# Kernel tuning notes

Hardware: AMD Instinct MI355X
Metric: run time of the kernel (lower is better)

## Reference

```python
import jax, jax.numpy as jnp
import numpy as np

B, T, N, C = 32, 12, 1024, 2   # batch, lookback window, n_series, in_channels
D, H, K, OUT = 16, 64, 2, 12   # embedding_dim, rnn_units, cheb_k, out_dim (horizon)


def setup_inputs() -> dict:
    key = jax.random.key(0)
    ks = jax.random.split(key, 12)
    p = lambda k, sh, s=0.1: jax.random.normal(k, sh, dtype=jnp.float32) * s
    return {
        "source": jax.random.normal(ks[0], (B, T, N, C), dtype=jnp.float32),
        "node_emb": p(ks[1], (N, D), 0.3),
        # layer 0: dim_in = C + H
        "gate_w0": p(ks[2], (D, K, C + H, 2 * H)),
        "gate_b0": p(ks[3], (D, 2 * H)),
        "upd_w0": p(ks[4], (D, K, C + H, H)),
        "upd_b0": p(ks[5], (D, H)),
        # layer 1: dim_in = H + H
        "gate_w1": p(ks[6], (D, K, 2 * H, 2 * H)),
        "gate_b1": p(ks[7], (D, 2 * H)),
        "upd_w1": p(ks[8], (D, K, 2 * H, H)),
        "upd_b1": p(ks[9], (D, H)),
        # end_conv: Conv2d(1, OUT*out_channels, kernel=(1,H)) == linear over hidden dim
        "conv_w": p(ks[10], (OUT, H)),
        "conv_b": p(ks[11], (OUT,)),
    }


def _supports(node_emb):
    # softmax(relu(E E^T)) row-normalized adaptive adjacency; Chebyshev stack (K, N, N)
    A = jax.nn.softmax(jax.nn.relu(node_emb @ node_emb.T), axis=1)
    s = [jnp.eye(N, dtype=A.dtype), A]
    for _ in range(2, K):
        s.append(2.0 * A @ s[-1] - s[-2])
    return jnp.stack(s, axis=0)


def _gcn(x, node_emb, w_pool, b_pool, supports):
    # x: (B, N, Cin); per-node adaptive weights from pools
    w = jnp.einsum('nd,dkio->nkio', node_emb, w_pool)     # (N, K, Cin, Cout)
    b = node_emb @ b_pool                                 # (N, Cout)
    xg = jnp.einsum('knm,bmc->bnkc', supports, x)         # (B, N, K, Cin)
    return jnp.einsum('bnki,nkio->bno', xg, w) + b


def _layer(x_seq, node_emb, supports, gw, gb, uw, ub):
    # x_seq: (B, T, N, Cin) -> (B, T, N, H) via GRU-style AGCRN cell, scanned over T
    def step(state, x_t):
        inp = jnp.concatenate([x_t, state], axis=-1)
        zr = jax.nn.sigmoid(_gcn(inp, node_emb, gw, gb, supports))
        z, r = jnp.split(zr, 2, axis=-1)
        cand = jnp.concatenate([x_t, z * state], axis=-1)
        hc = jnp.tanh(_gcn(cand, node_emb, uw, ub, supports))
        h = r * state + (1.0 - r) * hc
        return h, h

    init = jnp.zeros((x_seq.shape[0], N, H), dtype=x_seq.dtype)
    _, hs = jax.lax.scan(step, init, jnp.swapaxes(x_seq, 0, 1))
    return jnp.swapaxes(hs, 0, 1)


def reference(source, node_emb, gate_w0, gate_b0, upd_w0, upd_b0,
              gate_w1, gate_b1, upd_w1, upd_b1, conv_w, conv_b,
              teacher_forcing_ratio=0):
    sup = _supports(node_emb)  # adaptive supports depend only on static node_emb
    h1 = _layer(source, node_emb, sup, gate_w0, gate_b0, upd_w0, upd_b0)
    h2 = _layer(h1, node_emb, sup, gate_w1, gate_b1, upd_w1, upd_b1)
    last = h2[:, -1]  # (B, N, H)
    # end_conv over hidden dim -> (B, OUT, N); out_channels==1 so squeeze folds away
    out = jnp.einsum('bnh,oh->bon', last, conv_w) + conv_b[None, :, None]
    return out
```

## Files before the change

### kernel.cpp

```cpp
#include <hip/hip_runtime.h>
#include <hip/hip_fp16.h>


typedef _Float16 f16x8 __attribute__((ext_vector_type(8)));
typedef _Float16 f16x4 __attribute__((ext_vector_type(4)));
typedef float f32x4 __attribute__((ext_vector_type(4)));

#define WAIT_VM0 asm volatile("s_waitcnt vmcnt(0)" ::: "memory")
#define WAIT_VM1 asm volatile("s_waitcnt vmcnt(1)" ::: "memory")
#define WAIT_VM2 asm volatile("s_waitcnt vmcnt(2)" ::: "memory")
#define WAIT_VM1_LG asm volatile("s_waitcnt vmcnt(1) lgkmcnt(0)" ::: "memory")
#define WAIT_VM2_LG asm volatile("s_waitcnt vmcnt(2) lgkmcnt(0)" ::: "memory")
#define WAIT_LG asm volatile("s_waitcnt lgkmcnt(0)" ::: "memory")
#define BARRIER do { __builtin_amdgcn_s_barrier(); asm volatile("" ::: "memory"); } while (0)

__device__ __forceinline__ void gload_lds16(const void* g, void* l) {
  __builtin_amdgcn_global_load_lds(
      (const __attribute__((address_space(1))) void*)g,
      (__attribute__((address_space(3))) void*)l, 16, 0, 0);
}

__device__ __forceinline__ void dma_g128(const _Float16* Wc, _Float16* buf, int tid) {
  int wave = tid >> 6;
#pragma unroll
  for (int u = 0; u < 2; ++u) {
    gload_lds16(Wc + (size_t)(u * 256 + tid) * 8,
                buf + (size_t)(u * 256 + wave * 64) * 8);
  }
}

__device__ __forceinline__ void dma_g64(const _Float16* Wc, _Float16* buf, int tid) {
  int wave = tid >> 6;
  gload_lds16(Wc + (size_t)tid * 8, buf + (size_t)(wave * 64) * 8);
}

__device__ __forceinline__ f16x8 wrd(const _Float16* buf, int o, int s) {
  int flat = (o & 7) | (((s ^ (o & 3)) & 3) << 3) | ((o >> 3) << 5);
  return *(const f16x8*)(buf + flat * 8);
}

__global__ __launch_bounds__(256) void compute_A_kernel(const float* __restrict__ E,
                                                        __half* __restrict__ Ah) {
  int n = blockIdx.x;
  int tid = threadIdx.x;
  __shared__ float red[256];
  float en[16];
#pragma unroll
  for (int d = 0; d < 16; ++d) en[d] = E[n * 16 + d];
  float v[4];
#pragma unroll
  for (int q = 0; q < 4; ++q) {
    int m = tid + q * 256;
    const float* Em = E + m * 16;
    float dot = 0.f;
#pragma unroll
    for (int d = 0; d < 16; ++d) dot += en[d] * Em[d];
    v[q] = fmaxf(dot, 0.f);
  }
  float mx = fmaxf(fmaxf(v[0], v[1]), fmaxf(v[2], v[3]));
  red[tid] = mx; __syncthreads();
  for (int s = 128; s > 0; s >>= 1) { if (tid < s) red[tid] = fmaxf(red[tid], red[tid + s]); __syncthreads(); }
  mx = red[0];
  __syncthreads();
  float e[4], sum = 0.f;
#pragma unroll
  for (int q = 0; q < 4; ++q) { e[q] = expf(v[q] - mx); sum += e[q]; }
  red[tid] = sum; __syncthreads();
  for (int s = 128; s > 0; s >>= 1) { if (tid < s) red[tid] += red[tid + s]; __syncthreads(); }
  float inv = 1.f / red[0];
#pragma unroll
  for (int q = 0; q < 4; ++q) Ah[(size_t)n * 1024 + tid + q * 256] = __float2half(e[q] * inv);
}

__global__ __launch_bounds__(256) void pool_t16_kernel(const float* __restrict__ gw0,
                                                       const float* __restrict__ uw0,
                                                       const float* __restrict__ gw1,
                                                       const float* __restrict__ uw1,
                                                       __half* __restrict__ poolT16) {
  int rg = blockIdx.x;
  const float* pool; int F, Fp, O; size_t jbase; int kk, jj;
  if (rg < 160)      { pool = gw0; F = 66;  Fp = 80;  O = 128; jbase = 0;     kk = rg / 80;          jj = rg % 80; }
  else if (rg < 320) { pool = uw0; F = 66;  Fp = 80;  O = 64;  jbase = 20480; kk = (rg - 160) / 80;  jj = (rg - 160) % 80; }
  else if (rg < 576) { pool = gw1; F = 128; Fp = 128; O = 128; jbase = 30720; kk = (rg - 320) / 128; jj = (rg - 320) % 128; }
  else               { pool = uw1; F = 128; Fp = 128; O = 64;  jbase = 63488; kk = (rg - 576) / 128; jj = (rg - 576) % 128; }
  int o = threadIdx.x;
  if (o >= O) return;
  int i;
  if (F == Fp) i = jj;
  else i = (jj < 64) ? jj + 2 : (jj < 66 ? jj - 64 : -1);
  f16x8 a = {}, b = {}, zz = {};
  if (i >= 0) {
#pragma unroll
    for (int d = 0; d < 8; ++d)
      a[d] = (_Float16)pool[(((size_t)d * 2 + kk) * F + i) * O + o];
#pragma unroll
    for (int d = 8; d < 16; ++d)
      b[d - 8] = (_Float16)pool[(((size_t)d * 2 + kk) * F + i) * O + o];
  }
  size_t j = jbase + (size_t)o * (2 * Fp) + (size_t)kk * Fp + jj;
  _Float16* outp = (_Float16*)poolT16 + j * 32;
  *(f16x8*)outp = a;
  *(f16x8*)(outp + 8) = b;
  *(f16x8*)(outp + 16) = zz;
  *(f16x8*)(outp + 24) = zz;
}

__global__ __launch_bounds__(256) void prelude_misc_kernel(
    const float* __restrict__ E, __half* __restrict__ E16,
    const float* __restrict__ gb0, const float* __restrict__ ub0,
    const float* __restrict__ gb1, const float* __restrict__ ub1,
    float* __restrict__ Bg0, float* __restrict__ Bu0,
    float* __restrict__ Bg1, float* __restrict__ Bu1,
    const float* __restrict__ src, __half* __restrict__ x16,
    float4* __restrict__ zero_p) {
  int bid = blockIdx.x;
  if (bid < 8192) {
    int i = bid * 256 + threadIdx.x;
    zero_p[i] = float4{0.f, 0.f, 0.f, 0.f};
    return;
  }
  bid -= 8192;
  if (bid < 384) {
    int t0 = bid >> 5, b = bid & 31;
    const float* s = src + (size_t)(b * 12 + t0) * 2048;
    __half* dst = x16 + t0 * 64 + b * 2;
    for (int nn = threadIdx.x; nn < 1024; nn += 256) {
      float2 v = *(const float2*)(s + nn * 2);
      *(__half2*)(dst + (size_t)nn * 768) = __floats2half2_rn(v.x, v.y);
    }
    return;
  }
  bid -= 384;
  if (bid < 1536) {
    int tid = bid * 256 + threadIdx.x;
    if (tid >= 1024 * 384) return;
    int n = tid / 384, c = tid - n * 384;
    const float* pool; float* outp; int O, o;
    if (c < 128)      { pool = gb0; outp = Bg0; O = 128; o = c; }
    else if (c < 192) { pool = ub0; outp = Bu0; O = 64;  o = c - 128; }
    else if (c < 320) { pool = gb1; outp = Bg1; O = 128; o = c - 192; }
    else              { pool = ub1; outp = Bu1; O = 64;  o = c - 320; }
    const float* En = E + n * 16;
    float a = 0.f;
#pragma unroll
    for (int d = 0; d < 16; ++d) a += En[d] * pool[d * O + o];
    outp[n * O + o] = a;
    return;
  }
  bid -= 1536;
  {
    int t = bid * 256 + threadIdx.x;
    if (t >= 1024 * 32) return;
    int d = t & 31;
    E16[t] = (d < 16) ? __float2half(E[(t >> 5) * 16 + d]) : __half(0);
  }
}

__global__ __launch_bounds__(256) void make_wt_mfma_kernel(
    const __half* __restrict__ E16g, const __half* __restrict__ poolT16g,
    __half* __restrict__ WtG0, __half* __restrict__ WtU0,
    __half* __restrict__ WtG1, __half* __restrict__ WtU1) {
  __shared__ __align__(16) _Float16 Es[64][40];
  __shared__ __align__(16) _Float16 wbuf[64][264];
  const _Float16* E16 = (const _Float16*)E16g;
  const _Float16* pT = (const _Float16*)poolT16g;
  int bx = blockIdx.x;
  __half* Wt; int O, KIP, segbase, kc, og;
  if (bx < 80)       { Wt = WtG0; O = 128; KIP = 160; segbase = 0;     kc = bx % 5;          og = bx / 5; }
  else if (bx < 120) { Wt = WtU0; O = 64;  KIP = 160; segbase = 20480; kc = (bx - 80) % 5;   og = (bx - 80) / 5; }
  else if (bx < 248) { Wt = WtG1; O = 128; KIP = 256; segbase = 30720; kc = (bx - 120) % 8;  og = (bx - 120) / 8; }
  else               { Wt = WtU1; O = 64;  KIP = 256; segbase = 63488; kc = (bx - 248) % 8;  og = (bx - 248) / 8; }
  int o0 = og * 8;
  int n0 = blockIdx.y * 64;
  {
    int r = threadIdx.x >> 2, ch = (threadIdx.x & 3) * 8;
    *(f16x8*)&Es[r][ch] = *(const f16x8*)(E16 + (size_t)(n0 + r) * 32 + ch);
  }
  __syncthreads();
  int wave = threadIdx.x >> 6, lane = threadIdx.x & 63;
  int fm = lane & 15, fg = lane >> 4;
  f16x8 af[4];
#pragma unroll
  for (int i = 0; i < 4; ++i) af[i] = *(const f16x8*)&Es[i * 16 + fm][fg * 8];
  f32x4 acc[4][4] = {};
#pragma unroll
  for (int jt = 0; jt < 4; ++jt) {
    int local = wave * 64 + jt * 16 + fm;
    int oo = local >> 5, kip = local & 31;
    size_t jc = (size_t)segbase + (size_t)(o0 + oo) * KIP + kc * 32 + kip;
    f16x8 bf = *(const f16x8*)(pT + jc * 32 + fg * 8);
#pragma unroll
    for (int i = 0; i < 4; ++i)
      acc[i][jt] = __builtin_amdgcn_mfma_f32_16x16x32_f16(af[i], bf, acc[i][jt], 0, 0, 0);
  }
#pragma unroll
  for (int i = 0; i < 4; ++i)
#pragma unroll
    for (int jt = 0; jt < 4; ++jt)
#pragma unroll
      for (int r = 0; r < 4; ++r)
        wbuf[i * 16 + fg * 4 + r][wave * 64 + jt * 16 + fm] = (_Float16)acc[i][jt][r];
  __syncthreads();
  int NCH = KIP >> 5;
  int CH = O * 32;
  int sbase = (o0 >> 3) * 256;
  for (int idx = threadIdx.x; idx < 64 * 32; idx += 256) {
    int nsub = idx >> 5, w = idx & 31;
    int oo = w & 7;
    int s = (w >> 3) ^ (w & 3);
    int pos = oo * 32 + s * 8;
    size_t dst = ((size_t)(n0 + nsub) * NCH + kc) * CH + sbase + (size_t)w * 8;
    *(float4*)(Wt + dst) = *(float4*)&wbuf[nsub][pos];
  }
}

__global__ __launch_bounds__(256) void gemm_nt_kernel(
    const __half* __restrict__ Ahg, const __half* __restrict__ X0g,
    const __half* __restrict__ X1g, __half* __restrict__ Yg,
    int Nc, int cstride, int split) {
  __shared__ __align__(16) _Float16 As[64][136];
  __shared__ __align__(16) _Float16 Bs[64][144];
  const _Float16* __restrict__ Ah = (const _Float16*)Ahg;
  _Float16* __restrict__ Y = (_Float16*)Yg;
  int tid = threadIdx.x;
  int row0 = blockIdx.y * 64;
  int col0 = blockIdx.x * 64;
  const _Float16* __restrict__ Xsrc =
      (col0 < split) ? (const _Float16*)X0g : (const _Float16*)X1g;
  int colg = (col0 < split) ? col0 : col0 - split;
  int wave = tid >> 6, lane = tid & 63;
  int wm = wave & 1, wn = wave >> 1;
  int fm = lane & 15, fg = lane >> 4;

  int sr = tid >> 2, sc = (tid & 3) * 32;
  const _Float16* pa = Ah + (size_t)(row0 + sr) * 1024 + sc;
  int kq = tid & 31, cg = tid >> 5;
  int kb = 4 * kq;
  const _Float16* pb = Xsrc + (size_t)kb * cstride + colg + cg * 8;
  int chunk = kq >> 1;
  int kin = (kq & 1) * 4;

  f16x8 ra[4], rb[4];
#pragma unroll
  for (int c = 0; c < 4; ++c) ra[c] = *(const f16x8*)(pa + c * 8);
#pragma unroll
  for (int r = 0; r < 4; ++r) rb[r] = *(const f16x8*)(pb + (size_t)r * cstride);

  f32x4 acc[2][2] = {};
  for (int k0 = 0; k0 < 1024; k0 += 128) {
#pragma unroll
    for (int c = 0; c < 4; ++c) *(f16x8*)&As[sr][sc + c * 8] = ra[c];
#pragma unroll
    for (int i = 0; i < 8; ++i) {
      int c = cg * 8 + i;
// ... 68 lines not shown
  int kin = (kq & 1) * 4;

  f16x8 ra[4], rb[4][2];
#pragma unroll
  for (int c = 0; c < 4; ++c) ra[c] = *(const f16x8*)(pa + c * 8);
#pragma unroll
  for (int r = 0; r < 4; ++r)
#pragma unroll
    for (int h = 0; h < 2; ++h)
      rb[r][h] = *(const f16x8*)(pb + (size_t)r * cstride + h * 8);

  f32x4 acc[4][2] = {};
  for (int k0 = 0; k0 < 1024; k0 += 128) {
#pragma unroll
    for (int c = 0; c < 4; ++c) *(f16x8*)&As[sr][sc + c * 8] = ra[c];
#pragma unroll
    for (int h = 0; h < 2; ++h)
#pragma unroll
      for (int i = 0; i < 8; ++i) {
        int c = cg * 16 + h * 8 + i;
        f16x4 p;
        p[0] = rb[0][h][i]; p[1] = rb[1][h][i]; p[2] = rb[2][h][i]; p[3] = rb[3][h][i];
        *(f16x4*)&Bs[c][((chunk ^ (c & 7)) << 3) + kin] = p;
      }
    __syncthreads();
    if (k0 + 128 < 1024) {
#pragma unroll
      for (int c = 0; c < 4; ++c) ra[c] = *(const f16x8*)(pa + k0 + 128 + c * 8);
#pragma unroll
      for (int r = 0; r < 4; ++r)
#pragma unroll
        for (int h = 0; h < 2; ++h)
          rb[r][h] = *(const f16x8*)(pb + (size_t)(k0 + 128 + r) * cstride + h * 8);
    }
#pragma unroll
    for (int kc = 0; kc < 4; ++kc) {
      int ck = kc * 4 + fg;
      f16x8 af[4], bf[2];
#pragma unroll
      for (int i = 0; i < 4; ++i)
        af[i] = *(const f16x8*)&As[i * 16 + fm][kc * 32 + fg * 8];
#pragma unroll
      for (int j = 0; j < 2; ++j) {
        int cl = wave * 32 + j * 16 + fm;
        bf[j] = *(const f16x8*)&Bs[cl][(ck ^ (cl & 7)) << 3];
      }
#pragma unroll
      for (int i = 0; i < 4; ++i)
#pragma unroll
        for (int j = 0; j < 2; ++j)
          acc[i][j] = __builtin_amdgcn_mfma_f32_16x16x32_f16(af[i], bf[j], acc[i][j], 0, 0, 0);
    }
    __syncthreads();
  }
#pragma unroll
  for (int i = 0; i < 4; ++i) {
#pragma unroll
    for (int j = 0; j < 2; ++j) {
      int col = col0 + wave * 32 + j * 16 + fm;
      int rbase = row0 + i * 16 + fg * 4;
#pragma unroll
      for (int r = 0; r < 4; ++r)
        Y[(size_t)(rbase + r) * Nc + col] = (_Float16)acc[i][j][r];
    }
  }
}

__device__ __forceinline__ f16x8 ld_g0(const __half* __restrict__ h16,
                                       const __half* __restrict__ YBD, int n, int idx) {
  int b = idx >> 4, part = (idx >> 3) & 1, ch = idx & 7;
  const _Float16* s = part ? (const _Float16*)YBD + (size_t)n * 4096 + b * 64 + ch * 8
                           : (const _Float16*)h16 + (size_t)n * 2048 + b * 64 + ch * 8;
  return *(const f16x8*)s;
}
__device__ __forceinline__ f16x8 ld_u0(const __half* __restrict__ zh0,
                                       const __half* __restrict__ YCE, int n, int idx) {
  int b = idx >> 4, part = (idx >> 3) & 1, ch = idx & 7;
  const _Float16* s = part ? (const _Float16*)YCE + (size_t)n * 4096 + 2048 + b * 64 + ch * 8
                           : (const _Float16*)zh0 + (size_t)n * 2048 + b * 64 + ch * 8;
  return *(const f16x8*)s;
}

__device__ __forceinline__ void gate0_body(
    _Float16* Xs, _Float16 (*Wb)[4096], int n, int t,
    f16x8 pre0, f16x8 pre1, float2 xv, unsigned axu,
    const _Float16* Wn, const float* __restrict__ Bg,
    const float* __restrict__ h32, __half* __restrict__ zh0, __half* __restrict__ r0) {
  constexpr int STRIDE = 168;
  {
    int b0 = t >> 4, p0 = (t >> 3) & 1, c0 = t & 7;
    *(f16x8*)&Xs[b0 * STRIDE + p0 * 80 + c0 * 8] = pre0;
    int idx = t + 256;
    int b1 = idx >> 4, p1 = (idx >> 3) & 1, c1 = idx & 7;
    *(f16x8*)&Xs[b1 * STRIDE + p1 * 80 + c1 * 8] = pre1;
  }
  if (t < 32) {
    Xs[t * STRIDE + 64] = (_Float16)xv.x;
    Xs[t * STRIDE + 65] = (_Float16)xv.y;
    *(unsigned*)&Xs[t * STRIDE + 144] = axu;
  }
  for (int idx = t; idx < 896; idx += 256) {
    int b = idx / 28, jj = idx % 28;
    int col = (jj < 14) ? 66 + jj : 132 + jj;
    Xs[b * STRIDE + col] = (_Float16)0.f;
  }
  int wave = t >> 6, lane = t & 63;
  int fm = lane & 15, fg = lane >> 4;
  f32x4 acc[2][2] = {};
#pragma unroll
  for (int kc = 0; kc < 5; ++kc) {
    if (kc == 0) WAIT_VM2_LG;
    else if (kc < 4) WAIT_VM2;
    else WAIT_VM0;
    BARRIER;
    const _Float16* wb = Wb[kc & 1];
    f16x8 af[2], bf[2];
#pragma unroll
    for (int i = 0; i < 2; ++i)
      af[i] = *(const f16x8*)&Xs[(i * 16 + fm) * STRIDE + kc * 32 + fg * 8];
#pragma unroll
    for (int j = 0; j < 2; ++j)
      bf[j] = wrd(wb, wave * 32 + j * 16 + fm, fg);
    WAIT_LG;
    BARRIER;
    if (kc < 3) dma_g128(Wn + (size_t)(kc + 2) * 4096, Wb[kc & 1], t);
    __builtin_amdgcn_s_setprio(1);
#pragma unroll
    for (int i = 0; i < 2; ++i)
#pragma unroll
      for (int j = 0; j < 2; ++j)
        acc[i][j] = __builtin_amdgcn_mfma_f32_16x16x32_f16(af[i], bf[j], acc[i][j], 0, 0, 0);
    __builtin_amdgcn_s_setprio(0);
  }
  const float* Bn = Bg + n * 128;
#pragma unroll
  for (int j = 0; j < 2; ++j) {
    int o = wave * 32 + j * 16 + fm;
    float bias = Bn[o];
#pragma unroll
    for (int i = 0; i < 2; ++i)
#pragma unroll
      for (int r = 0; r < 4; ++r) {
        int b = i * 16 + fg * 4 + r;
        float s = 1.f / (1.f + __expf(-(acc[i][j][r] + bias)));
        size_t base = (size_t)n * 2048 + b * 64;
        if (o < 64) zh0[base + o] = __float2half(s * h32[base + o]);
        else        r0[base + o - 64] = __float2half(s);
      }
  }
}

__device__ __forceinline__ void upd0_body(
    _Float16* Xs, _Float16 (*Wb)[4096], int n, int t,
    f16x8 pre0, f16x8 pre1, float2 xv, unsigned axu,
    const _Float16* Wn, const float* __restrict__ Bu,
    const __half* __restrict__ r0, float* __restrict__ h32, __half* __restrict__ h16) {
  constexpr int STRIDE = 168;
  {
    int b0 = t >> 4, p0 = (t >> 3) & 1, c0 = t & 7;
    *(f16x8*)&Xs[b0 * STRIDE + p0 * 80 + c0 * 8] = pre0;
    int idx = t + 256;
    int b1 = idx >> 4, p1 = (idx >> 3) & 1, c1 = idx & 7;
    *(f16x8*)&Xs[b1 * STRIDE + p1 * 80 + c1 * 8] = pre1;
  }
  if (t < 32) {
    Xs[t * STRIDE + 64] = (_Float16)xv.x;
    Xs[t * STRIDE + 65] = (_Float16)xv.y;
    *(unsigned*)&Xs[t * STRIDE + 144] = axu;
  }
  for (int idx = t; idx < 896; idx += 256) {
    int b = idx / 28, jj = idx % 28;
    int col = (jj < 14) ? 66 + jj : 132 + jj;
    Xs[b * STRIDE + col] = (_Float16)0.f;
  }
  int wave = t >> 6, lane = t & 63;
  int fm = lane & 15, fg = lane >> 4;
  f32x4 acc[2] = {};
#pragma unroll
  for (int kc = 0; kc < 5; ++kc) {
    if (kc == 0) WAIT_VM1_LG;
    else if (kc < 4) WAIT_VM1;
    else WAIT_VM0;
    BARRIER;
    const _Float16* wb = Wb[kc & 1];
    f16x8 bf = wrd(wb, wave * 16 + fm, fg);
    f16x8 af0 = *(const f16x8*)&Xs[(0 * 16 + fm) * STRIDE + kc * 32 + fg * 8];
    f16x8 af1 = *(const f16x8*)&Xs[(1 * 16 + fm) * STRIDE + kc * 32 + fg * 8];
    WAIT_LG;
    BARRIER;
    if (kc < 3) dma_g64(Wn + (size_t)(kc + 2) * 2048, Wb[kc & 1], t);
    __builtin_amdgcn_s_setprio(1);
    acc[0] = __builtin_amdgcn_mfma_f32_16x16x32_f16(af0, bf, acc[0], 0, 0, 0);
    acc[1] = __builtin_amdgcn_mfma_f32_16x16x32_f16(af1, bf, acc[1], 0, 0, 0);
    __builtin_amdgcn_s_setprio(0);
  }
  int o = wave * 16 + fm;
  float bias = Bu[n * 64 + o];
#pragma unroll
  for (int i = 0; i < 2; ++i)
#pragma unroll
    for (int r = 0; r < 4; ++r) {
      int b = i * 16 + fg * 4 + r;
      float x = acc[i][r] + bias;
      x = fminf(fmaxf(x, -15.f), 15.f);
      float e = __expf(2.f * x);
      float hc = (e - 1.f) / (e + 1.f);
      size_t base = (size_t)n * 2048 + b * 64;
      float rr = __half2float(r0[base + o]);
      float hnew = rr * h32[base + o] + (1.f - rr) * hc;
      h32[base + o] = hnew;
      h16[base + o] = __float2half(hnew);
    }
}

__global__ __launch_bounds__(256) void gate0_kernel(
    const __half* __restrict__ h16, const __half* __restrict__ YBD,
    const float* __restrict__ src, const __half* __restrict__ Axt, int tstep,
    const __half* __restrict__ Wtg, const float* __restrict__ Bg,
    const float* __restrict__ h32, __half* __restrict__ zh0, __half* __restrict__ r0) {
  __shared__ __align__(16) _Float16 Xs[32 * 168];
  __shared__ __align__(16) _Float16 Wb[2][4096];
  int n = blockIdx.x, t = threadIdx.x;
  const _Float16* Wn = (const _Float16*)Wtg + (size_t)n * 20480;
  f16x8 p0 = ld_g0(h16, YBD, n, t);
  f16x8 p1 = ld_g0(h16, YBD, n, t + 256);
  float2 xv = {}; unsigned ax = 0;
  if (t < 32) {
    xv = *(const float2*)(src + ((size_t)(t * 12 + tstep) * 1024 + n) * 2);
    ax = *(const unsigned*)((const _Float16*)Axt + (size_t)n * 768 + tstep * 64 + t * 2);
  }
  dma_g128(Wn, Wb[0], t);
  dma_g128(Wn + 4096, Wb[1], t);
  gate0_body(Xs, Wb, n, t, p0, p1, xv, ax, Wn, Bg, h32, zh0, r0);
}

__global__ __launch_bounds__(256) void upd0_kernel(
    const __half* __restrict__ zh0, const __half* __restrict__ YCE,
    const float* __restrict__ src, const __half* __restrict__ Axt, int tstep,
    const __half* __restrict__ Wtg, const float* __restrict__ Bu,
    const __half* __restrict__ r0, float* __restrict__ h32, __half* __restrict__ h16) {
  __shared__ __align__(16) _Float16 Xs[32 * 168];
  __shared__ __align__(16) _Float16 Wb[2][4096];
  int n = blockIdx.x, t = threadIdx.x;
  const _Float16* Wn = (const _Float16*)Wtg + (size_t)n * 10240;
  f16x8 p0 = ld_u0(zh0, YCE, n, t);
  f16x8 p1 = ld_u0(zh0, YCE, n, t + 256);
  float2 xv = {}; unsigned ax = 0;
  if (t < 32) {
    xv = *(const float2*)(src + ((size_t)(t * 12 + tstep) * 1024 + n) * 2);
    ax = *(const unsigned*)((const _Float16*)Axt + (size_t)n * 768 + tstep * 64 + t * 2);
  }
  dma_g64(Wn, Wb[0], t);
  dma_g64(Wn + 2048, Wb[1], t);
  upd0_body(Xs, Wb, n, t, p0, p1, xv, ax, Wn, Bu, r0, h32, h16);
}

__global__ __launch_bounds__(256) void gate1_gate0_kernel(
    const __half* __restrict__ h1_16, const __half* __restrict__ h2_16,
    const __half* __restrict__ YBD,
    const __half* __restrict__ WtG1, const float* __restrict__ Bg1,
    const float* __restrict__ h2_32, __half* __restrict__ zh1, __half* __restrict__ r1,
    const float* __restrict__ src, const __half* __restrict__ Axt, int tnext,
    const __half* __restrict__ WtG0, const float* __restrict__ Bg0,
    const float* __restrict__ h1_32, __half* __restrict__ zh0, __half* __restrict__ r0,
    int do_gate0) {
  constexpr int STRIDE = 264;
  __shared__ __align__(16) _Float16 Xs[32 * STRIDE];
  __shared__ __align__(16) _Float16 Wb[2][4096];
  int n = blockIdx.x;
  int t = threadIdx.x;
  const _Float16* Wn1 = (const _Float16*)WtG1 + (size_t)n * 32768;
  const _Float16* Wn0 = (const _Float16*)WtG0 + (size_t)n * 20480;
  f16x8 s1[4];
#pragma unroll
  for (int u = 0; u < 4; ++u) {
    int idx = t + u * 256;
    int b = idx >> 5, q = idx & 31;
    const _Float16* s;
    if (q < 8)       s = (const _Float16*)h1_16 + (size_t)n * 2048 + b * 64 + q * 8;
    else if (q < 16) s = (const _Float16*)h2_16 + (size_t)n * 2048 + b * 64 + (q - 8) * 8;
    else if (q < 24) s = (const _Float16*)YBD + (size_t)n * 4096 + b * 64 + (q - 16) * 8;
    else             s = (const _Float16*)YBD + (size_t)n * 4096 + 2048 + b * 64 + (q - 24) * 8;
    s1[u] = *(const f16x8*)s;
  }
  f16x8 g0p0 = {}, g0p1 = {}; float2 g0xv = {}; unsigned g0ax = 0;
  if (do_gate0) {
    g0p0 = ld_g0(h1_16, YBD, n, t);
    g0p1 = ld_g0(h1_16, YBD, n, t + 256);
    if (t < 32) {
      g0xv = *(const float2*)(src + ((size_t)(t * 12 + tnext) * 1024 + n) * 2);
      g0ax = *(const unsigned*)((const _Float16*)Axt + (size_t)n * 768 + tnext * 64 + t * 2);
    }
  }
  dma_g128(Wn1, Wb[0], t);
  dma_g128(Wn1 + 4096, Wb[1], t);
#pragma unroll
  for (int u = 0; u < 4; ++u) {
    int idx = t + u * 256;
    int b = idx >> 5, q = idx & 31;
    *(f16x8*)&Xs[b * STRIDE + q * 8] = s1[u];
  }
  int wave = t >> 6, lane = t & 63;
  int fm = lane & 15, fg = lane >> 4;
  {
    f32x4 acc[2][2] = {};
#pragma unroll
    for (int kc = 0; kc < 8; ++kc) {
      if (kc == 0) WAIT_VM2_LG;
      else if (kc < 7) WAIT_VM2;
      else { if (do_gate0) WAIT_VM2; else WAIT_VM0; }
      BARRIER;
      const _Float16* wb = Wb[kc & 1];
      f16x8 af[2], bf[2];
#pragma unroll
      for (int i = 0; i < 2; ++i)
        af[i] = *(const f16x8*)&Xs[(i * 16 + fm) * STRIDE + kc * 32 + fg * 8];
#pragma unroll
      for (int j = 0; j < 2; ++j)
        bf[j] = wrd(wb, wave * 32 + j * 16 + fm, fg);
      WAIT_LG;
      BARRIER;
      if (kc < 6) dma_g128(Wn1 + (size_t)(kc + 2) * 4096, Wb[kc & 1], t);
      else if (do_gate0) dma_g128(Wn0 + (size_t)(kc - 6) * 4096, Wb[kc & 1], t);
      __builtin_amdgcn_s_setprio(1);
#pragma unroll
      for (int i = 0; i < 2; ++i)
#pragma unroll
        for (int j = 0; j < 2; ++j)
          acc[i][j] = __builtin_amdgcn_mfma_f32_16x16x32_f16(af[i], bf[j], acc[i][j], 0, 0, 0);
      __builtin_amdgcn_s_setprio(0);
    }
    const float* Bn = Bg1 + n * 128;
#pragma unroll
    for (int j = 0; j < 2; ++j) {
      int o = wave * 32 + j * 16 + fm;
      float bias = Bn[o];
#pragma unroll
      for (int i = 0; i < 2; ++i)
#pragma unroll
        for (int r = 0; r < 4; ++r) {
          int b = i * 16 + fg * 4 + r;
          float s = 1.f / (1.f + __expf(-(acc[i][j][r] + bias)));
          size_t base = (size_t)n * 2048 + b * 64;
          if (o < 64) zh1[base + o] = __float2half(s * h2_32[base + o]);
          else        r1[base + o - 64] = __float2half(s);
        }
    }
  }
  if (!do_gate0) return;
  gate0_body(Xs, Wb, n, t, g0p0, g0p1, g0xv, g0ax, Wn0, Bg0, h1_32, zh0, r0);
}

__global__ __launch_bounds__(256) void upd1_upd0_kernel(
    const __half* __restrict__ h1_16, const __half* __restrict__ zh1,
    const __half* __restrict__ YBD, const __half* __restrict__ YCE,
    const __half* __restrict__ WtU1, const float* __restrict__ Bu1,
    const __half* __restrict__ r1, float* __restrict__ h2_32, __half* __restrict__ h2_16,
    const __half* __restrict__ zh0,
    const float* __restrict__ src, const __half* __restrict__ Axt, int tnext,
    const __half* __restrict__ WtU0, const float* __restrict__ Bu0,
    const __half* __restrict__ r0, float* __restrict__ h1_32, __half* __restrict__ h1_16w,
    int do_upd0) {
  constexpr int STRIDE = 264;
  __shared__ __align__(16) _Float16 Xs[32 * STRIDE];
  __shared__ __align__(16) _Float16 Wb[2][4096];
  int n = blockIdx.x;
  int t = threadIdx.x;
  const _Float16* Wn1 = (const _Float16*)WtU1 + (size_t)n * 16384;
  const _Float16* Wn0 = (const _Float16*)WtU0 + (size_t)n * 10240;
  f16x8 s1[4];
#pragma unroll
  for (int u = 0; u < 4; ++u) {
    int idx = t + u * 256;
    int b = idx >> 5, q = idx & 31;
    const _Float16* s;
    if (q < 8)       s = (const _Float16*)h1_16 + (size_t)n * 2048 + b * 64 + q * 8;
    else if (q < 16) s = (const _Float16*)zh1 + (size_t)n * 2048 + b * 64 + (q - 8) * 8;
    else if (q < 24) s = (const _Float16*)YBD + (size_t)n * 4096 + b * 64 + (q - 16) * 8;
    else             s = (const _Float16*)YCE + (size_t)n * 4096 + b * 64 + (q - 24) * 8;
    s1[u] = *(const f16x8*)s;
  }
  f16x8 u0p0 = {}, u0p1 = {}; float2 u0xv = {}; unsigned u0ax = 0;
  if (do_upd0) {
    u0p0 = ld_u0(zh0, YCE, n, t);
    u0p1 = ld_u0(zh0, YCE, n, t + 256);
    if (t < 32) {
      u0xv = *(const float2*)(src + ((size_t)(t * 12 + tnext) * 1024 + n) * 2);
      u0ax = *(const unsigned*)((const _Float16*)Axt + (size_t)n * 768 + tnext * 64 + t * 2);
    }
  }
  dma_g64(Wn1, Wb[0], t);
  dma_g64(Wn1 + 2048, Wb[1], t);
#pragma unroll
  for (int u = 0; u < 4; ++u) {
    int idx = t + u * 256;
    int b = idx >> 5, q = idx & 31;
    *(f16x8*)&Xs[b * STRIDE + q * 8] = s1[u];
  }
  int wave = t >> 6, lane = t & 63;
  int fm = lane & 15, fg = lane >> 4;
  {
    f32x4 acc[2] = {};
#pragma unroll
    for (int kc = 0; kc < 8; ++kc) {
      if (kc == 0) WAIT_VM1_LG;
      else if (kc < 7) WAIT_VM1;
      else { if (do_upd0) WAIT_VM1; else WAIT_VM0; }
      BARRIER;
      const _Float16* wb = Wb[kc & 1];
      f16x8 bf = wrd(wb, wave * 16 + fm, fg);
      f16x8 af0 = *(const f16x8*)&Xs[(0 * 16 + fm) * STRIDE + kc * 32 + fg * 8];
      f16x8 af1 = *(const f16x8*)&Xs[(1 * 16 + fm) * STRIDE + kc * 32 + fg * 8];
      WAIT_LG;
      BARRIER;
      if (kc < 6) dma_g64(Wn1 + (size_t)(kc + 2) * 2048, Wb[kc & 1], t);
      else if (do_upd0) dma_g64(Wn0 + (size_t)(kc - 6) * 2048, Wb[kc & 1], t);
      __builtin_amdgcn_s_setprio(1);
      acc[0] = __builtin_amdgcn_mfma_f32_16x16x32_f16(af0, bf, acc[0], 0, 0, 0);
      acc[1] = __builtin_amdgcn_mfma_f32_16x16x32_f16(af1, bf, acc[1], 0, 0, 0);
      __builtin_amdgcn_s_setprio(0);
    }
    int o = wave * 16 + fm;
    float bias = Bu1[n * 64 + o];
#pragma unroll
    for (int i = 0; i < 2; ++i)
#pragma unroll
      for (int r = 0; r < 4; ++r) {
        int b = i * 16 + fg * 4 + r;
        float x = acc[i][r] + bias;
        x = fminf(fmaxf(x, -15.f), 15.f);
        float e = __expf(2.f * x);
        float hc = (e - 1.f) / (e + 1.f);
        size_t base = (size_t)n * 2048 + b * 64;
        float rr = __half2float(r1[base + o]);
        float hnew = rr * h2_32[base + o] + (1.f - rr) * hc;
        h2_32[base + o] = hnew;
        h2_16[base + o] = __float2half(hnew);
      }
  }
  if (!do_upd0) return;
  upd0_body(Xs, Wb, n, t, u0p0, u0p1, u0xv, u0ax, Wn0, Bu0, r0, h1_32, h1_16w);
}

__global__ void final_conv_kernel(const float* __restrict__ h2, const float* __restrict__ cw,
                                  const float* __restrict__ cb, float* __restrict__ out) {
  int tid = blockIdx.x * 256 + threadIdx.x;
  if (tid >= 32 * 1024) return;
  int n = tid & 1023, b = tid >> 10;
  const float* hp = h2 + ((size_t)n * 32 + b) * 64;
  float hv[64];
#pragma unroll
  for (int i = 0; i < 64; ++i) hv[i] = hp[i];
#pragma unroll
  for (int o = 0; o < 12; ++o) {
    float acc = cb[o];
#pragma unroll
    for (int i = 0; i < 64; ++i) acc += hv[i] * cw[o * 64 + i];
    out[((size_t)b * 12 + o) * 1024 + n] = acc;
  }
}

extern "C" void kernel_launch(void* const* d_in, const int* in_sizes, int n_in,
                              void* d_out, int out_size, void* d_ws, size_t ws_size,
                              hipStream_t stream) {
  const float* src = (const float*)d_in[0];
  const float* E   = (const float*)d_in[1];
  const float* gw0 = (const float*)d_in[2];
  const float* gb0 = (const float*)d_in[3];
  const float* uw0 = (const float*)d_in[4];
  const float* ub0 = (const float*)d_in[5];
  const float* gw1 = (const float*)d_in[6];
  const float* gb1 = (const float*)d_in[7];
  const float* uw1 = (const float*)d_in[8];
  const float* ub1 = (const float*)d_in[9];
  const float* cw  = (const float*)d_in[10];
  const float* cb  = (const float*)d_in[11];
  float* out = (float*)d_out;
  (void)in_sizes; (void)n_in; (void)out_size; (void)ws_size;

  char* base = (char*)d_ws;
  size_t off = 0;
  auto alloc = [&](size_t bytes) -> void* {
    void* p = base + off; off += (bytes + 511) & ~(size_t)511; return p;
  };
  __half* Ah   = (__half*)alloc((size_t)1024 * 1024 * 2);
  __half* WtG0 = (__half*)alloc((size_t)1024 * 128 * 160 * 2);
  __half* WtU0 = (__half*)alloc((size_t)1024 * 64 * 160 * 2);
  __half* WtG1 = (__half*)alloc((size_t)1024 * 128 * 256 * 2);
  __half* WtU1 = (__half*)alloc((size_t)1024 * 64 * 256 * 2);
  float*  Bg0  = (float*) alloc((size_t)1024 * 128 * 4);
  float*  Bu0  = (float*) alloc((size_t)1024 * 64 * 4);
  float*  Bg1  = (float*) alloc((size_t)1024 * 128 * 4);
  float*  Bu1  = (float*) alloc((size_t)1024 * 64 * 4);
  float*  h1_32 = (float*)alloc((size_t)1024 * 2048 * 4);
  float*  h2_32 = (float*)alloc((size_t)1024 * 2048 * 4);
  __half* h1_16 = (__half*)alloc((size_t)1024 * 2048 * 2);
  __half* h2_16 = (__half*)alloc((size_t)1024 * 2048 * 2);
  __half* YBD  = (__half*)alloc((size_t)1024 * 4096 * 2);
  __half* YCE  = (__half*)alloc((size_t)1024 * 4096 * 2);
  __half* zh0  = (__half*)alloc((size_t)1024 * 2048 * 2);
  __half* zh1  = (__half*)alloc((size_t)1024 * 2048 * 2);
  __half* Axt  = (__half*)alloc((size_t)1024 * 768 * 2);
  __half* r1   = (__half*)alloc((size_t)1024 * 2048 * 2);
  __half* r0   = (__half*)alloc((size_t)1024 * 2048 * 2);
  __half* poolT16 = (__half*)alloc((size_t)79872 * 32 * 2);
  __half* E16  = (__half*)alloc((size_t)1024 * 32 * 2);
  __half* x16  = (__half*)alloc((size_t)1024 * 768 * 2);

  compute_A_kernel<<<1024, 256, 0, stream>>>(E, Ah);
  prelude_misc_kernel<<<10240, 256, 0, stream>>>(E, E16, gb0, ub0, gb1, ub1,
                                                 Bg0, Bu0, Bg1, Bu1,
                                                 src, x16, (float4*)h1_32);
  pool_t16_kernel<<<832, 256, 0, stream>>>(gw0, uw0, gw1, uw1, poolT16);
  make_wt_mfma_kernel<<<dim3(312, 16), 256, 0, stream>>>(E16, poolT16, WtG0, WtU0, WtG1, WtU1);
  gemm_nt_kernel<<<dim3(12, 16), 256, 0, stream>>>(Ah, (__half*)x16, (__half*)x16, Axt,
                                                   768, 768, 768);

  gate0_kernel<<<1024, 256, 0, stream>>>(h1_16, YBD, src, Axt, 0, WtG0, Bg0, h1_32, zh0, r0);
  gemm_nt128_kernel<<<dim3(16, 16), 256, 0, stream>>>(Ah, zh0, zh0, YCE + 2048,
                                                      4096, 2048, 2048);
  upd0_kernel<<<1024, 256, 0, stream>>>(zh0, YCE, src, Axt, 0, WtU0, Bu0, r0, h1_32, h1_16);

  for (int t = 0; t < 12; ++t) {
    int more = (t < 11) ? 1 : 0;
    gemm_nt128_kernel<<<dim3(32, 16), 256, 0, stream>>>(Ah, h1_16, h2_16, YBD,
                                                        4096, 2048, 2048);
    gate1_gate0_kernel<<<1024, 256, 0, stream>>>(h1_16, h2_16, YBD, WtG1, Bg1, h2_32, zh1, r1,
                                                 src, Axt, t + 1, WtG0, Bg0, h1_32, zh0, r0,
                                                 more);
    gemm_nt128_kernel<<<dim3(32, 16), 256, 0, stream>>>(Ah, zh1, zh0, YCE,
                                                        4096, 2048, 2048);
    upd1_upd0_kernel<<<1024, 256, 0, stream>>>(h1_16, zh1, YBD, YCE, WtU1, Bu1, r1,
                                               h2_32, h2_16, zh0, src, Axt, t + 1,
                                               WtU0, Bu0, r0, h1_32, h1_16, more);
  }

  final_conv_kernel<<<(32 * 1024 + 255) / 256, 256, 0, stream>>>(h2_32, cw, cb, out);
}
```

Baseline: 1.343 ms.

## Split layer-0 input-channel terms out of MFMA into scalar epilogue FMAs

```diff
diff --git a/kernel.cpp b/kernel.cpp
--- a/kernel.cpp
+++ b/kernel.cpp
@@ -78,26 +78,21 @@
                                                        const float* __restrict__ uw1,
                                                        __half* __restrict__ poolT16) {
   int rg = blockIdx.x;
-  const float* pool; int F, Fp, O; size_t jbase; int kk, jj;
-  if (rg < 160)      { pool = gw0; F = 66;  Fp = 80;  O = 128; jbase = 0;     kk = rg / 80;          jj = rg % 80; }
-  else if (rg < 320) { pool = uw0; F = 66;  Fp = 80;  O = 64;  jbase = 20480; kk = (rg - 160) / 80;  jj = (rg - 160) % 80; }
-  else if (rg < 576) { pool = gw1; F = 128; Fp = 128; O = 128; jbase = 30720; kk = (rg - 320) / 128; jj = (rg - 320) % 128; }
-  else               { pool = uw1; F = 128; Fp = 128; O = 64;  jbase = 63488; kk = (rg - 576) / 128; jj = (rg - 576) % 128; }
+  const float* pool; int F, O, TK; size_t jb; int kk, jj, i;
+  if (rg < 128)      { pool = gw0; F = 66;  O = 128; TK = 64;  jb = 0;     kk = rg >> 6; jj = rg & 63; i = jj + 2; }
+  else if (rg < 256) { int r = rg - 128; pool = uw0; F = 66;  O = 64;  TK = 64;  jb = 16384; kk = r >> 6; jj = r & 63;  i = jj + 2; }
+  else if (rg < 512) { int r = rg - 256; pool = gw1; F = 128; O = 128; TK = 128; jb = 24576; kk = r >> 7; jj = r & 127; i = jj; }
+  else               { int r = rg - 512; pool = uw1; F = 128; O = 64;  TK = 128; jb = 57344; kk = r >> 7; jj = r & 127; i = jj; }
   int o = threadIdx.x;
   if (o >= O) return;
-  int i;
-  if (F == Fp) i = jj;
-  else i = (jj < 64) ? jj + 2 : (jj < 66 ? jj - 64 : -1);
-  f16x8 a = {}, b = {}, zz = {};
-  if (i >= 0) {
-#pragma unroll
-    for (int d = 0; d < 8; ++d)
-      a[d] = (_Float16)pool[(((size_t)d * 2 + kk) * F + i) * O + o];
-#pragma unroll
-    for (int d = 8; d < 16; ++d)
-      b[d - 8] = (_Float16)pool[(((size_t)d * 2 + kk) * F + i) * O + o];
-  }
-  size_t j = jbase + (size_t)o * (2 * Fp) + (size_t)kk * Fp + jj;
+  f16x8 a, b, zz = {};
+#pragma unroll
+  for (int d = 0; d < 8; ++d)
+    a[d] = (_Float16)pool[(((size_t)d * 2 + kk) * F + i) * O + o];
+#pragma unroll
+  for (int d = 8; d < 16; ++d)
+    b[d - 8] = (_Float16)pool[(((size_t)d * 2 + kk) * F + i) * O + o];
+  size_t j = jb + (size_t)o * (2 * TK) + (size_t)kk * TK + jj;
   _Float16* outp = (_Float16*)poolT16 + j * 32;
   *(f16x8*)outp = a;
   *(f16x8*)(outp + 8) = b;
@@ -112,6 +107,8 @@
     float* __restrict__ Bg0, float* __restrict__ Bu0,
     float* __restrict__ Bg1, float* __restrict__ Bu1,
     const float* __restrict__ src, __half* __restrict__ x16,
+    const float* __restrict__ gw0, const float* __restrict__ uw0,
+    float* __restrict__ WxG0, float* __restrict__ WxU0,
     float4* __restrict__ zero_p) {
   int bid = blockIdx.x;
   if (bid < 8192) {
@@ -148,11 +145,36 @@
     return;
   }
   bid -= 1536;
-  {
+  if (bid < 128) {
     int t = bid * 256 + threadIdx.x;
-    if (t >= 1024 * 32) return;
     int d = t & 31;
     E16[t] = (d < 16) ? __float2half(E[(t >> 5) * 16 + d]) : __half(0);
+    return;
+  }
+  bid -= 128;
+  if (bid < 2048) {
+    int v = bid * 256 + threadIdx.x;
+    int n = v >> 9, q = (v >> 7) & 3, o = v & 127;
+    int kk = q >> 1, c = q & 1;
+    const float* En = E + n * 16;
+    float a = 0.f;
+#pragma unroll
+    for (int d = 0; d < 16; ++d)
+      a += En[d] * gw0[(((size_t)d * 2 + kk) * 66 + c) * 128 + o];
+    WxG0[(size_t)n * 512 + q * 128 + o] = __half2float(__float2half(a));
+    return;
+  }
+  bid -= 2048;
+  {
+    int v = bid * 256 + threadIdx.x;
+    int n = v >> 8, q = (v >> 6) & 3, o = v & 63;
+    int kk = q >> 1, c = q & 1;
+    const float* En = E + n * 16;
+    float a = 0.f;
+#pragma unroll
+    for (int d = 0; d < 16; ++d)
+      a += En[d] * uw0[(((size_t)d * 2 + kk) * 66 + c) * 64 + o];
+    WxU0[(size_t)n * 256 + q * 64 + o] = __half2float(__float2half(a));
   }
 }
 
@@ -166,10 +188,10 @@
   const _Float16* pT = (const _Float16*)poolT16g;
   int bx = blockIdx.x;
   __half* Wt; int O, KIP, segbase, kc, og;
-  if (bx < 80)       { Wt = WtG0; O = 128; KIP = 160; segbase = 0;     kc = bx % 5;          og = bx / 5; }
-  else if (bx < 120) { Wt = WtU0; O = 64;  KIP = 160; segbase = 20480; kc = (bx - 80) % 5;   og = (bx - 80) / 5; }
-  else if (bx < 248) { Wt = WtG1; O = 128; KIP = 256; segbase = 30720; kc = (bx - 120) % 8;  og = (bx - 120) / 8; }
-  else               { Wt = WtU1; O = 64;  KIP = 256; segbase = 63488; kc = (bx - 248) % 8;  og = (bx - 248) / 8; }
+  if (bx < 64)       { Wt = WtG0; O = 128; KIP = 128; segbase = 0;     kc = bx & 3;  og = bx >> 2; }
+  else if (bx < 96)  { int b = bx - 64;  Wt = WtU0; O = 64;  KIP = 128; segbase = 16384; kc = b & 3; og = b >> 2; }
+  else if (bx < 224) { int b = bx - 96;  Wt = WtG1; O = 128; KIP = 256; segbase = 24576; kc = b & 7; og = b >> 3; }
+  else               { int b = bx - 224; Wt = WtU1; O = 64;  KIP = 256; segbase = 57344; kc = b & 7; og = b >> 3; }
   int o0 = og * 8;
   int n0 = blockIdx.y * 64;
   {
@@ -404,35 +426,32 @@
 }
 
 __device__ __forceinline__ void gate0_body(
-    _Float16* Xs, _Float16 (*Wb)[4096], int n, int t,
+    _Float16* Xs, float (*xq)[4], _Float16 (*Wb)[4096], int n, int t,
     f16x8 pre0, f16x8 pre1, float2 xv, unsigned axu,
-    const _Float16* Wn, const float* __restrict__ Bg,
+    const _Float16* Wn, const float* __restrict__ Bg, const float* __restrict__ Wxg,
     const float* __restrict__ h32, __half* __restrict__ zh0, __half* __restrict__ r0) {
-  constexpr int STRIDE = 168;
+  constexpr int STRIDE = 136;
   {
     int b0 = t >> 4, p0 = (t >> 3) & 1, c0 = t & 7;
-    *(f16x8*)&Xs[b0 * STRIDE + p0 * 80 + c0 * 8] = pre0;
+    *(f16x8*)&Xs[b0 * STRIDE + p0 * 64 + c0 * 8] = pre0;
     int idx = t + 256;
     int b1 = idx >> 4, p1 = (idx >> 3) & 1, c1 = idx & 7;
-    *(f16x8*)&Xs[b1 * STRIDE + p1 * 80 + c1 * 8] = pre1;
+    *(f16x8*)&Xs[b1 * STRIDE + p1 * 64 + c1 * 8] = pre1;
   }
   if (t < 32) {
-    Xs[t * STRIDE + 64] = (_Float16)xv.x;
-    Xs[t * STRIDE + 65] = (_Float16)xv.y;
-    *(unsigned*)&Xs[t * STRIDE + 144] = axu;
-  }
-  for (int idx = t; idx < 896; idx += 256) {
-    int b = idx / 28, jj = idx % 28;
-    int col = (jj < 14) ? 66 + jj : 132 + jj;
-    Xs[b * STRIDE + col] = (_Float16)0.f;
+    __half2 ah = *(__half2*)&axu;
+    float2 af2 = __half22float2(ah);
+    xq[t][0] = __half2float(__float2half(xv.x));
+    xq[t][1] = __half2float(__float2half(xv.y));
+    xq[t][2] = af2.x; xq[t][3] = af2.y;
   }
   int wave = t >> 6, lane = t & 63;
   int fm = lane & 15, fg = lane >> 4;
   f32x4 acc[2][2] = {};
 #pragma unroll
-  for (int kc = 0; kc < 5; ++kc) {
+  for (int kc = 0; kc < 4; ++kc) {
     if (kc == 0) WAIT_VM2_LG;
-    else if (kc < 4) WAIT_VM2;
+    else if (kc < 3) WAIT_VM2;
     else WAIT_VM0;
     BARRIER;
     const _Float16* wb = Wb[kc & 1];
@@ -445,7 +464,7 @@
       bf[j] = wrd(wb, wave * 32 + j * 16 + fm, fg);
     WAIT_LG;
     BARRIER;
-    if (kc < 3) dma_g128(Wn + (size_t)(kc + 2) * 4096, Wb[kc & 1], t);
+    if (kc < 2) dma_g128(Wn + (size_t)(kc + 2) * 4096, Wb[kc & 1], t);
     __builtin_amdgcn_s_setprio(1);
 #pragma unroll
     for (int i = 0; i < 2; ++i)
@@ -455,16 +474,20 @@
     __builtin_amdgcn_s_setprio(0);
   }
   const float* Bn = Bg + n * 128;
+  const float* Wx = Wxg + (size_t)n * 512;
 #pragma unroll
   for (int j = 0; j < 2; ++j) {
     int o = wave * 32 + j * 16 + fm;
     float bias = Bn[o];
+    float w0 = Wx[o], w1 = Wx[128 + o], w2 = Wx[256 + o], w3 = Wx[384 + o];
 #pragma unroll
     for (int i = 0; i < 2; ++i)
 #pragma unroll
       for (int r = 0; r < 4; ++r) {
         int b = i * 16 + fg * 4 + r;
-        float s = 1.f / (1.f + __expf(-(acc[i][j][r] + bias)));
+        float px = acc[i][j][r] + bias +
+                   w0 * xq[b][0] + w1 * xq[b][1] + w2 * xq[b][2] + w3 * xq[b][3];
+        float s = 1.f / (1.f + __expf(-px));
         size_t base = (size_t)n * 2048 + b * 64;
         if (o < 64) zh0[base + o] = __float2half(s * h32[base + o]);
         else        r0[base + o - 64] = __float2half(s);
@@ -473,35 +496,32 @@
 }
 
 __device__ __forceinline__ void upd0_body(
-    _Float16* Xs, _Float16 (*Wb)[4096], int n, int t,
+    _Float16* Xs, float (*xq)[4], _Float16 (*Wb)[2048], int n, int t,
     f16x8 pre0, f16x8 pre1, float2 xv, unsigned axu,
-    const _Float16* Wn, const float* __restrict__ Bu,
+    const _Float16* Wn, const float* __restrict__ Bu, const float* __restrict__ Wxu,
     const __half* __restrict__ r0, float* __restrict__ h32, __half* __restrict__ h16) {
-  constexpr int STRIDE = 168;
+  constexpr int STRIDE = 136;
   {
     int b0 = t >> 4, p0 = (t >> 3) & 1, c0 = t & 7;
-    *(f16x8*)&Xs[b0 * STRIDE + p0 * 80 + c0 * 8] = pre0;
+    *(f16x8*)&Xs[b0 * STRIDE + p0 * 64 + c0 * 8] = pre0;
     int idx = t + 256;
     int b1 = idx >> 4, p1 = (idx >> 3) & 1, c1 = idx & 7;
-    *(f16x8*)&Xs[b1 * STRIDE + p1 * 80 + c1 * 8] = pre1;
+    *(f16x8*)&Xs[b1 * STRIDE + p1 * 64 + c1 * 8] = pre1;
   }
   if (t < 32) {
-    Xs[t * STRIDE + 64] = (_Float16)xv.x;
-    Xs[t * STRIDE + 65] = (_Float16)xv.y;
-    *(unsigned*)&Xs[t * STRIDE + 144] = axu;
-  }
-  for (int idx = t; idx < 896; idx += 256) {
-    int b = idx / 28, jj = idx % 28;
-    int col = (jj < 14) ? 66 + jj : 132 + jj;
-    Xs[b * STRIDE + col] = (_Float16)0.f;
+    __half2 ah = *(__half2*)&axu;
+    float2 af2 = __half22float2(ah);
+    xq[t][0] = __half2float(__float2half(xv.x));
+    xq[t][1] = __half2float(__float2half(xv.y));
+    xq[t][2] = af2.x; xq[t][3] = af2.y;
   }
   int wave = t >> 6, lane = t & 63;
   int fm = lane & 15, fg = lane >> 4;
   f32x4 acc[2] = {};
 #pragma unroll
-  for (int kc = 0; kc < 5; ++kc) {
+  for (int kc = 0; kc < 4; ++kc) {
     if (kc == 0) WAIT_VM1_LG;
-    else if (kc < 4) WAIT_VM1;
+    else if (kc < 3) WAIT_VM1;
     else WAIT_VM0;
     BARRIER;
     const _Float16* wb = Wb[kc & 1];
@@ -510,7 +530,7 @@
     f16x8 af1 = *(const f16x8*)&Xs[(1 * 16 + fm) * STRIDE + kc * 32 + fg * 8];
     WAIT_LG;
     BARRIER;
-    if (kc < 3) dma_g64(Wn + (size_t)(kc + 2) * 2048, Wb[kc & 1], t);
+    if (kc < 2) dma_g64(Wn + (size_t)(kc + 2) * 2048, Wb[kc & 1], t);
     __builtin_amdgcn_s_setprio(1);
     acc[0] = __builtin_amdgcn_mfma_f32_16x16x32_f16(af0, bf, acc[0], 0, 0, 0);
     acc[1] = __builtin_amdgcn_mfma_f32_16x16x32_f16(af1, bf, acc[1], 0, 0, 0);
@@ -518,12 +538,15 @@
   }
   int o = wave * 16 + fm;
   float bias = Bu[n * 64 + o];
+  const float* Wx = Wxu + (size_t)n * 256;
+  float w0 = Wx[o], w1 = Wx[64 + o], w2 = Wx[128 + o], w3 = Wx[192 + o];
 #pragma unroll
   for (int i = 0; i < 2; ++i)
 #pragma unroll
     for (int r = 0; r < 4; ++r) {
       int b = i * 16 + fg * 4 + r;
-      float x = acc[i][r] + bias;
+      float x = acc[i][r] + bias +
+                w0 * xq[b][0] + w1 * xq[b][1] + w2 * xq[b][2] + w3 * xq[b][3];
       x = fminf(fmaxf(x, -15.f), 15.f);
       float e = __expf(2.f * x);
       float hc = (e - 1.f) / (e + 1.f);
@@ -539,11 +562,13 @@
     const __half* __restrict__ h16, const __half* __restrict__ YBD,
     const float* __restrict__ src, const __half* __restrict__ Axt, int tstep,
     const __half* __restrict__ Wtg, const float* __restrict__ Bg,
+    const float* __restrict__ Wxg,
     const float* __restrict__ h32, __half* __restrict__ zh0, __half* __restrict__ r0) {
-  __shared__ __align__(16) _Float16 Xs[32 * 168];
+  __shared__ __align__(16) _Float16 Xs[32 * 136];
   __shared__ __align__(16) _Float16 Wb[2][4096];
+  __shared__ float xq[32][4];
   int n = blockIdx.x, t = threadIdx.x;
-  const _Float16* Wn = (const _Float16*)Wtg + (size_t)n * 20480;
+  const _Float16* Wn = (const _Float16*)Wtg + (size_t)n * 16384;
   f16x8 p0 = ld_g0(h16, YBD, n, t);
   f16x8 p1 = ld_g0(h16, YBD, n, t + 256);
   float2 xv = {}; unsigned ax = 0;
@@ -553,18 +578,20 @@
   }
   dma_g128(Wn, Wb[0], t);
   dma_g128(Wn + 4096, Wb[1], t);
-  gate0_body(Xs, Wb, n, t, p0, p1, xv, ax, Wn, Bg, h32, zh0, r0);
+  gate0_body(Xs, xq, Wb, n, t, p0, p1, xv, ax, Wn, Bg, Wxg, h32, zh0, r0);
 }
 
 __global__ __launch_bounds__(256) void upd0_kernel(
     const __half* __restrict__ zh0, const __half* __restrict__ YCE,
     const float* __restrict__ src, const __half* __restrict__ Axt, int tstep,
     const __half* __restrict__ Wtg, const float* __restrict__ Bu,
+    const float* __restrict__ Wxu,
     const __half* __restrict__ r0, float* __restrict__ h32, __half* __restrict__ h16) {
-  __shared__ __align__(16) _Float16 Xs[32 * 168];
-  __shared__ __align__(16) _Float16 Wb[2][4096];
+  __shared__ __align__(16) _Float16 Xs[32 * 136];
+  __shared__ __align__(16) _Float16 Wb[2][2048];
+  __shared__ float xq[32][4];
   int n = blockIdx.x, t = threadIdx.x;
-  const _Float16* Wn = (const _Float16*)Wtg + (size_t)n * 10240;
+  const _Float16* Wn = (const _Float16*)Wtg + (size_t)n * 8192;
   f16x8 p0 = ld_u0(zh0, YCE, n, t);
   f16x8 p1 = ld_u0(zh0, YCE, n, t + 256);
   float2 xv = {}; unsigned ax = 0;
@@ -574,7 +601,7 @@
   }
   dma_g64(Wn, Wb[0], t);
   dma_g64(Wn + 2048, Wb[1], t);
-  upd0_body(Xs, Wb, n, t, p0, p1, xv, ax, Wn, Bu, r0, h32, h16);
+  upd0_body(Xs, xq, Wb, n, t, p0, p1, xv, ax, Wn, Bu, Wxu, r0, h32, h16);
 }
 
 __global__ __launch_bounds__(256) void gate1_gate0_kernel(
@@ -584,15 +611,17 @@
     const float* __restrict__ h2_32, __half* __restrict__ zh1, __half* __restrict__ r1,
     const float* __restrict__ src, const __half* __restrict__ Axt, int tnext,
     const __half* __restrict__ WtG0, const float* __restrict__ Bg0,
+    const float* __restrict__ WxG0,
     const float* __restrict__ h1_32, __half* __restrict__ zh0, __half* __restrict__ r0,
     int do_gate0) {
   constexpr int STRIDE = 264;
   __shared__ __align__(16) _Float16 Xs[32 * STRIDE];
   __shared__ __align__(16) _Float16 Wb[2][4096];
+  __shared__ float xq[32][4];
   int n = blockIdx.x;
   int t = threadIdx.x;
   const _Float16* Wn1 = (const _Float16*)WtG1 + (size_t)n * 32768;
-  const _Float16* Wn0 = (const _Float16*)WtG0 + (size_t)n * 20480;
+  const _Float16* Wn0 = (const _Float16*)WtG0 + (size_t)n * 16384;
   f16x8 s1[4];
 #pragma unroll
   for (int u = 0; u < 4; ++u) {
@@ -670,7 +699,7 @@
     }
   }
   if (!do_gate0) return;
-  gate0_body(Xs, Wb, n, t, g0p0, g0p1, g0xv, g0ax, Wn0, Bg0, h1_32, zh0, r0);
+  gate0_body(Xs, xq, Wb, n, t, g0p0, g0p1, g0xv, g0ax, Wn0, Bg0, WxG0, h1_32, zh0, r0);
 }
 
 __global__ __launch_bounds__(256) void upd1_upd0_kernel(
@@ -681,15 +710,17 @@
     const __half* __restrict__ zh0,
     const float* __restrict__ src, const __half* __restrict__ Axt, int tnext,
     const __half* __restrict__ WtU0, const float* __restrict__ Bu0,
+    const float* __restrict__ WxU0,
     const __half* __restrict__ r0, float* __restrict__ h1_32, __half* __restrict__ h1_16w,
     int do_upd0) {
   constexpr int STRIDE = 264;
   __shared__ __align__(16) _Float16 Xs[32 * STRIDE];
-  __shared__ __align__(16) _Float16 Wb[2][4096];
+  __shared__ __align__(16) _Float16 Wb[2][2048];
+  __shared__ float xq[32][4];
   int n = blockIdx.x;
   int t = threadIdx.x;
   const _Float16* Wn1 = (const _Float16*)WtU1 + (size_t)n * 16384;
-  const _Float16* Wn0 = (const _Float16*)WtU0 + (size_t)n * 10240;
+  const _Float16* Wn0 = (const _Float16*)WtU0 + (size_t)n * 8192;
   f16x8 s1[4];
 #pragma unroll
   for (int u = 0; u < 4; ++u) {
@@ -761,7 +792,7 @@
       }
   }
   if (!do_upd0) return;
-  upd0_body(Xs, Wb, n, t, u0p0, u0p1, u0xv, u0ax, Wn0, Bu0, r0, h1_32, h1_16w);
+  upd0_body(Xs, xq, Wb, n, t, u0p0, u0p1, u0xv, u0ax, Wn0, Bu0, WxU0, r0, h1_32, h1_16w);
 }
 
 __global__ void final_conv_kernel(const float* __restrict__ h2, const float* __restrict__ cw,
@@ -806,14 +837,16 @@
     void* p = base + off; off += (bytes + 511) & ~(size_t)511; return p;
   };
   __half* Ah   = (__half*)alloc((size_t)1024 * 1024 * 2);
-  __half* WtG0 = (__half*)alloc((size_t)1024 * 128 * 160 * 2);
-  __half* WtU0 = (__half*)alloc((size_t)1024 * 64 * 160 * 2);
+  __half* WtG0 = (__half*)alloc((size_t)1024 * 128 * 128 * 2);
+  __half* WtU0 = (__half*)alloc((size_t)1024 * 64 * 128 * 2);
   __half* WtG1 = (__half*)alloc((size_t)1024 * 128 * 256 * 2);
   __half* WtU1 = (__half*)alloc((size_t)1024 * 64 * 256 * 2);
   float*  Bg0  = (float*) alloc((size_t)1024 * 128 * 4);
   float*  Bu0  = (float*) alloc((size_t)1024 * 64 * 4);
   float*  Bg1  = (float*) alloc((size_t)1024 * 128 * 4);
   float*  Bu1  = (float*) alloc((size_t)1024 * 64 * 4);
+  float*  WxG0 = (float*) alloc((size_t)1024 * 512 * 4);
+  float*  WxU0 = (float*) alloc((size_t)1024 * 256 * 4);
   float*  h1_32 = (float*)alloc((size_t)1024 * 2048 * 4);
   float*  h2_32 = (float*)alloc((size_t)1024 * 2048 * 4);
   __half* h1_16 = (__half*)alloc((size_t)1024 * 2048 * 2);
@@ -825,36 +858,39 @@
   __half* Axt  = (__half*)alloc((size_t)1024 * 768 * 2);
   __half* r1   = (__half*)alloc((size_t)1024 * 2048 * 2);
   __half* r0   = (__half*)alloc((size_t)1024 * 2048 * 2);
-  __half* poolT16 = (__half*)alloc((size_t)79872 * 32 * 2);
+  __half* poolT16 = (__half*)alloc((size_t)73728 * 32 * 2);
   __half* E16  = (__half*)alloc((size_t)1024 * 32 * 2);
   __half* x16  = (__half*)alloc((size_t)1024 * 768 * 2);
 
   compute_A_kernel<<<1024, 256, 0, stream>>>(E, Ah);
-  prelude_misc_kernel<<<10240, 256, 0, stream>>>(E, E16, gb0, ub0, gb1, ub1,
+  prelude_misc_kernel<<<13312, 256, 0, stream>>>(E, E16, gb0, ub0, gb1, ub1,
                                                  Bg0, Bu0, Bg1, Bu1,
-                                                 src, x16, (float4*)h1_32);
-  pool_t16_kernel<<<832, 256, 0, stream>>>(gw0, uw0, gw1, uw1, poolT16);
-  make_wt_mfma_kernel<<<dim3(312, 16), 256, 0, stream>>>(E16, poolT16, WtG0, WtU0, WtG1, WtU1);
+                                                 src, x16, gw0, uw0, WxG0, WxU0,
+                                                 (float4*)h1_32);
+  pool_t16_kernel<<<768, 256, 0, stream>>>(gw0, uw0, gw1, uw1, poolT16);
+  make_wt_mfma_kernel<<<dim3(288, 16), 256, 0, stream>>>(E16, poolT16, WtG0, WtU0, WtG1, WtU1);
   gemm_nt_kernel<<<dim3(12, 16), 256, 0, stream>>>(Ah, (__half*)x16, (__half*)x16, Axt,
                                                    768, 768, 768);
 
-  gate0_kernel<<<1024, 256, 0, stream>>>(h1_16, YBD, src, Axt, 0, WtG0, Bg0, h1_32, zh0, r0);
+  gate0_kernel<<<1024, 256, 0, stream>>>(h1_16, YBD, src, Axt, 0, WtG0, Bg0, WxG0,
+                                         h1_32, zh0, r0);
   gemm_nt128_kernel<<<dim3(16, 16), 256, 0, stream>>>(Ah, zh0, zh0, YCE + 2048,
                                                       4096, 2048, 2048);
-  upd0_kernel<<<1024, 256, 0, stream>>>(zh0, YCE, src, Axt, 0, WtU0, Bu0, r0, h1_32, h1_16);
+  upd0_kernel<<<1024, 256, 0, stream>>>(zh0, YCE, src, Axt, 0, WtU0, Bu0, WxU0,
+                                        r0, h1_32, h1_16);
 
   for (int t = 0; t < 12; ++t) {
     int more = (t < 11) ? 1 : 0;
     gemm_nt128_kernel<<<dim3(32, 16), 256, 0, stream>>>(Ah, h1_16, h2_16, YBD,
                                                         4096, 2048, 2048);
     gate1_gate0_kernel<<<1024, 256, 0, stream>>>(h1_16, h2_16, YBD, WtG1, Bg1, h2_32, zh1, r1,
-                                                 src, Axt, t + 1, WtG0, Bg0, h1_32, zh0, r0,
-                                                 more);
+                                                 src, Axt, t + 1, WtG0, Bg0, WxG0,
+                                                 h1_32, zh0, r0, more);
     gemm_nt128_kernel<<<dim3(32, 16), 256, 0, stream>>>(Ah, zh1, zh0, YCE,
                                                         4096, 2048, 2048);
     upd1_upd0_kernel<<<1024, 256, 0, stream>>>(h1_16, zh1, YBD, YCE, WtU1, Bu1, r1,
                                                h2_32, h2_16, zh0, src, Axt, t + 1,
-                                               WtU0, Bu0, r0, h1_32, h1_16, more);
+                                               WtU0, Bu0, WxU0, r0, h1_32, h1_16, more);
   }
 
   final_conv_kernel<<<(32 * 1024 + 255) / 256, 256, 0, stream>>>(h2_32, cw, cb, out);
```

Result: no change. 1.324 ms (-1.4%).
